# Kernel tuning notes

Hardware: AMD Instinct MI355X
Metric: run time of the kernel (lower is better)

Reference implementation:

```python
import jax, jax.numpy as jnp
import numpy as np

C = 512
NUM_GROUPS = 4
EPS = 1e-6


def _conv1x1(W, b, t):
    # 1x1x1 Conv3d == per-position linear over channels
    return jnp.einsum('oc,bcfhw->bofhw', W, t) + b[None, :, None, None, None]


def setup_inputs() -> dict:
    key = jax.random.key(0)
    ks = jax.random.split(key, 11)
    c = C
    x = jax.random.normal(ks[0], (12, c, 48, 48), dtype=jnp.float32)
    p = lambda k: jax.random.normal(k, (c, c), dtype=jnp.float32) * 0.02
    return {
        'x': x,
        'norm_scale': jnp.ones((c,), jnp.float32),
        'norm_bias': jnp.zeros((c,), jnp.float32),
        'q_w': p(ks[1]), 'q_b': jnp.zeros((c,), jnp.float32),
        'k_w': p(ks[2]), 'k_b': jnp.zeros((c,), jnp.float32),
        'v_w': p(ks[3]), 'v_b': jnp.zeros((c,), jnp.float32),
        'proj_w': p(ks[4]), 'proj_b': jnp.zeros((c,), jnp.float32),
    }


def reference(x, norm_scale, norm_bias, q_w, q_b, k_w, k_b, v_w, v_b, proj_w, proj_b):
    b3, c, h, w = x.shape
    b = b3 // 3
    # chunk batch into 3 frames, stack at frame dim -> (b, c, 3, h, w)
    h_ = jnp.stack(jnp.split(x, 3, axis=0), axis=2)
    # GroupNorm(num_groups=4) over (C/G, F, H, W) per group
    g = NUM_GROUPS
    xg = h_.reshape(b, g, c // g, 3, h, w)
    mean = jnp.mean(xg, axis=(2, 3, 4, 5), keepdims=True)
    var = jnp.var(xg, axis=(2, 3, 4, 5), keepdims=True)
    xn = ((xg - mean) * jax.lax.rsqrt(var + EPS)).reshape(b, c, 3, h, w)
    hn = xn * norm_scale[None, :, None, None, None] + norm_bias[None, :, None, None, None]
    q = _conv1x1(q_w, q_b, hn)[:, :, 1:2]          # middle frame only: (b,c,1,h,w)
    skip = q[:, :, 0]                               # (b,c,h,w)
    k = _conv1x1(k_w, k_b, hn)                      # (b,c,3,h,w)
    v = _conv1x1(v_w, v_b, hn)
    n = h * w
    qf = q.reshape(b, c, n)                         # (b,c,n)
    kf = k.reshape(b, c, 3 * n)                     # (b,c,3n)
    vf = v.reshape(b, c, 3 * n)
    scores = jnp.einsum('bcn,bcm->bnm', qf, kf) * (float(c) ** -0.5)
    attn = jax.nn.softmax(scores, axis=2)           # (b,n,3n)
    out = jnp.einsum('bcm,bnm->bcn', vf, attn).reshape(b, c, 1, h, w)
    out = _conv1x1(proj_w, proj_b, out)[:, :, 0]
    return skip + out
```

## Files before the change

kernel.cpp:

```cpp
#include <hip/hip_runtime.h>

typedef unsigned short u16;
typedef unsigned long long u64;
typedef __attribute__((ext_vector_type(8))) short short8;
typedef __attribute__((ext_vector_type(4))) float f32x4;

__device__ __forceinline__ float bf2f(u16 h) {
    union { unsigned int u; float f; } v; v.u = ((unsigned int)h) << 16; return v.f;
}
__device__ __forceinline__ u16 f2bf(float f) {
    union { float f; unsigned int u; } v; v.f = f;
    unsigned int r = v.u + 0x7fffu + ((v.u >> 16) & 1u);
    return (u16)(r >> 16);
}

__device__ __forceinline__ void gload16(const u16* g, u16* l) {
    __builtin_amdgcn_global_load_lds(
        (const __attribute__((address_space(1))) void*)g,
        (__attribute__((address_space(3))) void*)l,
        16, 0, 0);
}

__device__ __forceinline__ float waveSum(float v) {
#pragma unroll
    for (int o = 32; o > 0; o >>= 1) v += __shfl_down(v, o);
    return v;
}
__device__ __forceinline__ float waveMax(float v) {
#pragma unroll
    for (int o = 32; o > 0; o >>= 1) v = fmaxf(v, __shfl_down(v, o));
    return v;
}
__device__ __forceinline__ int waveSumI(int v) {
#pragma unroll
    for (int o = 32; o > 0; o >>= 1) v += __shfl_down(v, o);
    return v;
}

__global__ __launch_bounds__(256) void detect_k(const u16* __restrict__ x, int* __restrict__ flag) {
    __shared__ int cnt[4];
    int c = 0;
    for (int i = threadIdx.x; i < 8192; i += 256) {
        u16 e = x[i * 2];
        int ex = (e >> 7) & 0xFF;
        c += (ex == 0 || (ex >= 100 && ex <= 150)) ? 1 : 0;
    }
    c = waveSumI(c);
    if ((threadIdx.x & 63) == 0) cnt[threadIdx.x >> 6] = c;
    __syncthreads();
    if (threadIdx.x == 0)
        flag[0] = ((cnt[0] + cnt[1] + cnt[2] + cnt[3]) > 4915) ? 1 : 0;
}

__global__ __launch_bounds__(256) void conv_k(const void* __restrict__ src, u16* __restrict__ dst,
                                              int n8, const int* __restrict__ flag) {
    int i = blockIdx.x * 256 + threadIdx.x;
    if (i >= n8) return;
    if (flag[0]) {
        ((int4*)dst)[i] = ((const int4*)src)[i];
    } else {
        const float* f = (const float*)src + (size_t)i * 8;
        union { int4 v4; u16 o[8]; } tv;
#pragma unroll
        for (int j = 0; j < 8; j++) tv.o[j] = f2bf(f[j]);
        ((int4*)dst)[i] = tv.v4;
    }
}

__global__ __launch_bounds__(256) void conv_w4(const void* s0, const void* s1, const void* s2, const void* s3,
                                               u16* __restrict__ dst, const int* __restrict__ flag) {
    int i = blockIdx.x * 256 + threadIdx.x;
    int w = blockIdx.y;
    const void* s = w == 0 ? s0 : w == 1 ? s1 : w == 2 ? s2 : s3;
    u16* d = dst + (size_t)w * 262144;
    if (flag[0]) {
        ((int4*)d)[i] = ((const int4*)s)[i];
    } else {
        const float* f = (const float*)s + (size_t)i * 8;
        union { int4 v4; u16 o[8]; } tv;
#pragma unroll
        for (int j = 0; j < 8; j++) tv.o[j] = f2bf(f[j]);
        ((int4*)d)[i] = tv.v4;
    }
}

__global__ __launch_bounds__(256) void conv_v6(const void* s0, const void* s1, const void* s2,
                                               const void* s3, const void* s4, const void* s5,
                                               u16* __restrict__ dst, const int* __restrict__ flag) {
    for (int i = threadIdx.x; i < 384; i += 256) {
        int seg = i >> 6, off = i & 63;
        const void* s = seg == 0 ? s0 : seg == 1 ? s1 : seg == 2 ? s2 : seg == 3 ? s3 : seg == 4 ? s4 : s5;
        u16* d = dst + (size_t)seg * 512;
        if (flag[0]) {
            ((int4*)d)[off] = ((const int4*)s)[off];
        } else {
            const float* f = (const float*)s + (size_t)off * 8;
            union { int4 v4; u16 o[8]; } tv;
#pragma unroll
            for (int j = 0; j < 8; j++) tv.o[j] = f2bf(f[j]);
            ((int4*)d)[off] = tv.v4;
        }
    }
}

__global__ __launch_bounds__(256) void gn_stats(const u16* __restrict__ x, float* __restrict__ stat) {
    __shared__ float red[8];
    const int gg = blockIdx.y, chunk = blockIdx.x;
    const int b = gg >> 2, g = gg & 3;
    float s = 0.f, s2 = 0.f;
    for (int pp = 0; pp < 12; pp++) {
        int p = chunk * 12 + pp;
        int t = p >> 7, cc = p & 127;
        const u16* rowp = x + (size_t)((t * 4 + b) * 512 + g * 128 + cc) * 2304;
        for (int vi = threadIdx.x; vi < 288; vi += 256) {
            union { int4 v4; u16 u[8]; } tv;
            tv.v4 = *(const int4*)(rowp + vi * 8);
#pragma unroll
            for (int j = 0; j < 8; j++) { float f = bf2f(tv.u[j]); s += f; s2 += f * f; }
        }
    }
    s = waveSum(s); s2 = waveSum(s2);
    int wid = threadIdx.x >> 6;
    if ((threadIdx.x & 63) == 0) { red[wid] = s; red[wid + 4] = s2; }
    __syncthreads();
    if (threadIdx.x == 0) {
        atomicAdd(&stat[gg], red[0] + red[1] + red[2] + red[3]);
        atomicAdd(&stat[16 + gg], red[4] + red[5] + red[6] + red[7]);
    }
}

__global__ void gn_ab(const float* __restrict__ stat, const u16* __restrict__ scale,
                      const u16* __restrict__ bias, float2* __restrict__ ab) {
    int idx = blockIdx.x * 256 + threadIdx.x;
    int b = idx >> 9, c = idx & 511, g = c >> 7, gg = b * 4 + g;
    const float invN = 1.f / 884736.f;
    float mean = stat[gg] * invN;
    float var  = stat[16 + gg] * invN - mean * mean;
    float rstd = rsqrtf(var + 1e-6f);
    float a = rstd * bf2f(scale[c]);
    ab[idx] = make_float2(a, bf2f(bias[c]) - mean * a);
}

__global__ __launch_bounds__(256) void normT_k(const u16* __restrict__ xb,
                                               const float2* __restrict__ ab,
                                               u16* __restrict__ xnT) {
    __shared__ u16 t[64][72];
    const int zz = blockIdx.z;
    const int b = zz & 3, tt = zz >> 2;
    const u16* s = xb + (size_t)zz * 512 * 2304;
    u16* d = xnT + (size_t)b * (512L * 6912) + (size_t)tt * 2304 * 512;
    const int c0 = blockIdx.x * 64;
    const int r0 = blockIdx.y * 64;
    const int tid = threadIdx.x;
#pragma unroll
    for (int p = 0; p < 4; p++) {
        int r = p * 16 + (tid >> 4);
        int c4 = (tid & 15) * 4;
        float2 sab = ab[b * 512 + r0 + r];
        union { u64 u; u16 e[4]; } tv;
        tv.u = *(const u64*)(s + (size_t)(r0 + r) * 2304 + c0 + c4);
#pragma unroll
        for (int j = 0; j < 4; j++) t[r][c4 + j] = f2bf(bf2f(tv.e[j]) * sab.x + sab.y);
    }
    __syncthreads();
#pragma unroll
    for (int p = 0; p < 2; p++) {
        int n = p * 32 + (tid >> 3);
        int c8 = (tid & 7) * 8;
        union { int4 v4; u16 o[8]; } tv;
#pragma unroll
        for (int j = 0; j < 8; j++) tv.o[j] = t[c8 + j][n];
        *(int4*)(d + (size_t)(c0 + n) * 512 + r0 + c8) = tv.v4;
    }
}

template<int WR, int WC, int TI, int TJ, int AMODE, int BMODE, int EPI, int F32OUT, int SPLITK, int SWZ>
__global__ __launch_bounds__(256)
void gemm_k(const u16* __restrict__ A, const u16* __restrict__ B, void* __restrict__ Cv,
            const u16* __restrict__ bias, const u16* __restrict__ skip,
            const float2* __restrict__ ab,
            int lda, int ldb, int ldc,
            int K, float alpha, int m_off, int b0,
            long aZS, long bZS, long cZS, long sZS) {
    constexpr int BM = WR * TI * 16;
    constexpr int BN = WC * TJ * 16;
    constexpr int LDA_S = (AMODE == 0) ? 32 : 44;
    constexpr int LDB_S = (BMODE == 1) ? 32 : 44;
    __shared__ alignas(16) u16 As[2][BM][LDA_S];
    __shared__ alignas(16) u16 Bs[2][BN][LDB_S];

    int bxi = blockIdx.x, byi = blockIdx.y, bzi = blockIdx.z;
    if (SWZ) {
        int gx = gridDim.x, gy = gridDim.y;
        long NN = (long)gx * gy * gridDim.z;
        long L = bxi + (long)gx * (byi + (long)gy * bzi);
        long q = NN >> 3, r = NN & 7;
        long xc = L & 7, m = L >> 3;
        long nl = (xc < r ? xc * (q + 1) : r * (q + 1) + (xc - r) * q) + m;
        bxi = (int)(nl % gx);
        long t2 = nl / gx;
        byi = (int)(t2 % gy);
        bzi = (int)(t2 / gy);
    }

    const int tid = threadIdx.x;
    const int z = bzi;
    const int i0b = byi * BM;
    const int j0b = bxi * BN;
    const int kstart = SPLITK ? z * K : 0;

    const u16* Ap = A + (size_t)z * aZS;
    const u16* Bp;
    const float2* abp = nullptr;
    int yx0 = 0;
    if (BMODE == 2) {
        int b = b0 + (SPLITK ? 0 : z);
        int m_tile = j0b + m_off;
        int t = m_tile / 2304;
        yx0 = m_tile - t * 2304;
        Bp = B + (size_t)((t * 4 + b) * 512) * 2304;
        abp = ab + b * 512;
    } else {
        Bp = B + (size_t)z * bZS;
    }
    const u16* Sp = (EPI & 10) ? (skip + (size_t)z * sZS) : nullptr;
    float* Cf = (float*)Cv + (size_t)z * (F32OUT ? cZS : 0);
    u16*   Ch = (u16*)Cv   + (size_t)z * (F32OUT ? 0 : cZS);

    const int wave = tid >> 6;
    const int lane = tid & 63;
    const int wr = wave / WC;
    const int wc = wave % WC;
    const int lrow = lane & 15;
    const int quad = lane >> 4;
    const int sws = ((quad ^ ((lrow >> 1) & 3)) << 3);

    auto stage = [&](int bsel, int k0) {
        if (AMODE == 0) {
            constexpr int NV = (BM * 32 / 8) / 256;
#pragma unroll
            for (int v = 0; v < NV; v++) {
                int vid = tid + v * 256;
                int i = vid >> 2;
                int ks = (((vid & 3) ^ ((vid >> 3) & 3)) * 8);
                gload16(Ap + (size_t)(i0b + i) * lda + (k0 + ks), &As[bsel][i][(vid & 3) * 8]);
            }
        } else {
            constexpr int NV = (BM * 32 / 8) / 256;
            constexpr int IG = BM / 8;
#pragma unroll
            for (int v = 0; v < NV; v++) {
                int vid = tid + v * 256;
                int k = vid / IG, ib = (vid % IG) * 8;
                union { int4 v4; u16 s[8]; } tv;
                tv.v4 = *(const int4*)(Ap + (size_t)(k0 + k) * lda + (i0b + ib));
#pragma unroll
                for (int j = 0; j < 8; j++) As[bsel][ib + j][k] = tv.s[j];
            }
        }
        if (BMODE == 1) {
            constexpr int NV = (BN * 32 / 8) / 256;
#pragma unroll
            for (int v = 0; v < NV; v++) {
                int vid = tid + v * 256;
                int j = vid >> 2;
                int ks = (((vid & 3) ^ ((vid >> 3) & 3)) * 8);
                gload16(Bp + (size_t)(j0b + j) * ldb + (k0 + ks), &Bs[bsel][j][(vid & 3) * 8]);
            }
        } else {
            constexpr int NV = (BN * 32 / 8) / 256;
            constexpr int JG = BN / 8;
#pragma unroll
            for (int v = 0; v < NV; v++) {
                int vid = tid + v * 256;
                int k = vid / JG, jb = (vid % JG) * 8;
                if (BMODE == 0) {
                    union { int4 v4; u16 s[8]; } tv;
                    tv.v4 = *(const int4*)(Bp + (size_t)(k0 + k) * ldb + (j0b + jb));
#pragma unroll
                    for (int j = 0; j < 8; j++) Bs[bsel][jb + j][k] = tv.s[j];
                } else {
                    union { int4 v4; u16 s[8]; } tv;
                    tv.v4 = *(const int4*)(Bp + (size_t)(k0 + k) * 2304 + (yx0 + jb));
                    float2 amb = abp[k0 + k];
#pragma unroll
                    for (int j = 0; j < 8; j++)
                        Bs[bsel][jb + j][k] = f2bf(bf2f(tv.s[j]) * amb.x + amb.y);
                }
            }
        }
    };

    f32x4 acc[TI][TJ] = {};
    const int kend = kstart + K;

    stage(0, kstart);
    __syncthreads();

    int cur = 0;
    for (int k0 = kstart; k0 < kend; k0 += 32) {
        if (k0 + 32 < kend) stage(cur ^ 1, k0 + 32);

        union FragU { short8 v; u64 u[2]; int4 v4; };
        FragU fa[TI], fb[TJ];
#pragma unroll
        for (int ri = 0; ri < TI; ri++) {
            int r = wr * TI * 16 + ri * 16 + lrow;
            if constexpr (LDA_S == 32) {
                fa[ri].v4 = *(const int4*)(&As[cur][r][sws]);
            } else {
                fa[ri].u[0] = *(const u64*)(&As[cur][r][quad * 8]);
                fa[ri].u[1] = *(const u64*)(&As[cur][r][quad * 8 + 4]);
            }
        }
#pragma unroll
        for (int cj = 0; cj < TJ; cj++) {
            int cc2 = wc * TJ * 16 + cj * 16 + lrow;
            if constexpr (LDB_S == 32) {
                fb[cj].v4 = *(const int4*)(&Bs[cur][cc2][sws]);
            } else {
                fb[cj].u[0] = *(const u64*)(&Bs[cur][cc2][quad * 8]);
                fb[cj].u[1] = *(const u64*)(&Bs[cur][cc2][quad * 8 + 4]);
            }
        }
#pragma unroll
        for (int ri = 0; ri < TI; ri++)
#pragma unroll
            for (int cj = 0; cj < TJ; cj++)
                acc[ri][cj] = __builtin_amdgcn_mfma_f32_16x16x32_bf16(
                    fa[ri].v, fb[cj].v, acc[ri][cj], 0, 0, 0);

        __syncthreads();
        cur ^= 1;
    }

#pragma unroll
    for (int ri = 0; ri < TI; ri++) {
#pragma unroll
        for (int reg = 0; reg < 4; reg++) {
            int gi = i0b + wr * TI * 16 + ri * 16 + quad * 4 + reg;
            float bv = (EPI & 1) ? bf2f(bias[gi]) : 0.f;
#pragma unroll
            for (int cj = 0; cj < TJ; cj++) {
                int gj = j0b + wc * TJ * 16 + cj * 16 + lrow;
                float v = acc[ri][cj][reg] * alpha + bv;
                if (EPI & 4) v += bf2f(bias[gj]);
                if (EPI & 2) v += bf2f(Sp[(size_t)gi * ldc + gj]);
                if (EPI & 8) v += bf2f(Sp[(size_t)gj * 512 + gi]);
                if (F32OUT) Cf[(size_t)gi * ldc + gj] = v;
                else        Ch[(size_t)gi * ldc + gj] = f2bf(v);
            }
        }
    }
}

__global__ __launch_bounds__(256) void softmax_k(u16* __restrict__ sb, long zs) {
    __shared__ float row[6912];
    __shared__ float red[8];
    u16* p = sb + (size_t)blockIdx.y * zs + (size_t)blockIdx.x * 6912;
    const int tid = threadIdx.x;
    float mx = -3.0e38f;
    for (int vi = tid; vi < 864; vi += 256) {
        union { int4 v4; u16 u[8]; } tv;
        tv.v4 = *(const int4*)(p + vi * 8);
#pragma unroll
        for (int j = 0; j < 8; j++) { float f = bf2f(tv.u[j]); row[vi * 8 + j] = f; mx = fmaxf(mx, f); }
    }
    mx = waveMax(mx);
    if ((tid & 63) == 0) red[tid >> 6] = mx;
    __syncthreads();
    mx = fmaxf(fmaxf(red[0], red[1]), fmaxf(red[2], red[3]));
    __syncthreads();
    float sum = 0.f;
    for (int i = tid; i < 6912; i += 256) {
        float e = __expf(row[i] - mx);
        row[i] = e; sum += e;
    }
    sum = waveSum(sum);
    if ((tid & 63) == 0) red[4 + (tid >> 6)] = sum;
    __syncthreads();
    float inv = 1.f / (red[4] + red[5] + red[6] + red[7]);
    for (int vi = tid; vi < 864; vi += 256) {
        union { int4 v4; u16 u[8]; } tv;
#pragma unroll
        for (int j = 0; j < 8; j++) tv.u[j] = f2bf(row[vi * 8 + j] * inv);
        *(int4*)(p + vi * 8) = tv.v4;
    }
}

extern "C" void kernel_launch(void* const* d_in, const int* in_sizes, int n_in,
                              void* d_out, int out_size, void* d_ws, size_t ws_size,
                              hipStream_t stream) {
    float* out = (float*)d_out;

    const long QS = (long)512 * 2304;
    const long KS = (long)512 * 6912;
    const long SS = (long)2304 * 6912;
    const long PS = (long)512 * 2304;
    const float rs = 0.044194173824159216f;

    const size_t FIXED = 256 + 256 + 2048 * sizeof(float2)
                       + (size_t)14155776 * 2 + (size_t)4 * 262144 * 2 + 8192
                       + (size_t)14155776 * 2;
    const size_t PERNB = (size_t)(QS + KS + KS + QS + SS) * 2;
    int nb = 0;
    if      (ws_size >= FIXED + 4 * PERNB) nb = 4;
    else if (ws_size >= FIXED + 2 * PERNB) nb = 2;
    else if (ws_size >= FIXED + 1 * PERNB) nb = 1;

    char* w = (char*)d_ws;
    int*    flag = (int*)w;     w += 256;
    float*  stat = (float*)w;   w += 256;
    float2* ab   = (float2*)w;  w += 2048 * sizeof(float2);
    u16* xb = (u16*)w;  w += (size_t)14155776 * 2;
    u16* wgt = (u16*)w; w += (size_t)4 * 262144 * 2;
    u16* vecb = (u16*)w; w += 8192;

    detect_k<<<1, 256, 0, stream>>>((const u16*)d_in[0], flag);
    conv_k<<<6912, 256, 0, stream>>>(d_in[0], xb, 1769472, flag);
    conv_w4<<<dim3(128, 4), 256, 0, stream>>>(d_in[3], d_in[5], d_in[7], d_in[9], wgt, flag);
    conv_v6<<<1, 256, 0, stream>>>(d_in[1], d_in[2], d_in[4], d_in[6], d_in[8], d_in[10], vecb, flag);
    hipMemsetAsync(stat, 0, 32 * sizeof(float), stream);
    gn_stats<<<dim3(32, 16), 256, 0, stream>>>(xb, stat);
    gn_ab<<<8, 256, 0, stream>>>(stat, vecb, vecb + 512, ab);

    const u16* qw = wgt;
    const u16* kw = wgt + 262144;
    const u16* vw = wgt + 2 * 262144;
    const u16* pw = wgt + 3 * 262144;
    const u16* qb2 = vecb + 1024, *kb2 = vecb + 1536, *vb2 = vecb + 2048, *pb2 = vecb + 2560;

    if (nb == 0) {
        u16* qbuf = (u16*)w;  w += QS * 2;
        u16* kbuf = (u16*)w;  w += KS * 2;
        u16* vbuf = (u16*)w;  w += KS * 2;
        u16* obuf = (u16*)w;  w += QS * 2;
        u16* sbuf = (u16*)w;
        for (int b = 0; b < 4; b++) {
            gemm_k<2,2,4,4,0,2,1,0,0,0><<<dim3(54,4,1),256,0,stream>>>(
                kw, xb, kbuf, kb2, nullptr, ab, 512,0,6912, 512,1.f,0,b, 0,0,0,0);
            gemm_k<2,2,4,4,0,2,1,0,0,0><<<dim3(54,4,1),256,0,stream>>>(
                vw, xb, vbuf, vb2, nullptr, ab, 512,0,6912, 512,1.f,0,b, 0,0,0,0);
            gemm_k<2,2,4,4,0,2,1,0,0,0><<<dim3(18,4,1),256,0,stream>>>(
                qw, xb, qbuf, qb2, nullptr, ab, 512,0,2304, 512,1.f,2304,b, 0,0,0,0);
            gemm_k<2,2,4,4,1,0,0,0,0,0><<<dim3(54,18,1),256,0,stream>>>(
                qbuf, kbuf, sbuf, nullptr,nullptr,nullptr, 2304,6912,6912, 512,rs,0,b, 0,0,0,0);
            softmax_k<<<dim3(2304,1),256,0,stream>>>(sbuf, 0);
            gemm_k<1,4,4,1,0,1,0,0,0,0><<<dim3(36,8,1),256,0,stream>>>(
                vbuf, sbuf, obuf, nullptr,nullptr,nullptr, 6912,6912,2304, 6912,1.f,0,b, 0,0,0,0);
            gemm_k<2,2,4,2,0,0,3,1,0,0><<<dim3(36,4,1),256,0,stream>>>(
                pw, obuf, out + (size_t)b * PS, pb2, qbuf, nullptr,
                512,2304,2304, 512,1.f,0,b, 0,0,0,0);
        }
        return;
    }

    u16* xnT = (u16*)w; w += (size_t)14155776 * 2;
    u16* qT  = (u16*)w; w += (size_t)nb * QS * 2;
    u16* kT  = (u16*)w; w += (size_t)nb * KS * 2;
    u16* vbuf= (u16*)w; w += (size_t)nb * KS * 2;
    u16* obT = (u16*)w; w += (size_t)nb * QS * 2;
    u16* sbuf= (u16*)w; w += (size_t)nb * SS * 2;

    normT_k<<<dim3(36, 8, 12), 256, 0, stream>>>(xb, ab, xnT);

    for (int g = 0; g < 4; g += nb) {
        gemm_k<2,2,4,4,0,1,4,0,0,1><<<dim3(4,54,nb),256,0,stream>>>(
            xnT + (size_t)g * KS, kw, kT, kb2, nullptr, nullptr,
            512,512,512, 512,1.f,0,g, KS,0,KS,0);
        gemm_k<2,2,4,4,0,1,4,0,0,1><<<dim3(4,18,nb),256,0,stream>>>(
            xnT + (size_t)g * KS + (size_t)2304 * 512, qw, qT, qb2, nullptr, nullptr,
            512,512,512, 512,1.f,0,g, KS,0,QS,0);
        gemm_k<2,2,4,4,0,1,1,0,0,1><<<dim3(54,4,nb),256,0,stream>>>(
            vw, xnT + (size_t)g * KS, vbuf, vb2, nullptr, nullptr,
            512,512,6912, 512,1.f,0,g, 0,KS,KS,0);
        gemm_k<2,2,4,4,0,1,0,0,0,1><<<dim3(54,18,nb),256,0,stream>>>(
            qT, kT, sbuf, nullptr,nullptr,nullptr, 512,512,6912, 512,rs,0,g, QS,KS,SS,0);
        softmax_k<<<dim3(2304,nb),256,0,stream>>>(sbuf, SS);
        gemm_k<2,2,2,4,0,1,0,0,0,1><<<dim3(4,36,nb),256,0,stream>>>(
            sbuf, vbuf, obT, nullptr,nullptr,nullptr, 6912,6912,512, 6912,1.f,0,g, SS,KS,QS,0);
        gemm_k<2,2,4,2,0,1,9,1,0,1><<<dim3(36,4,nb),256,0,stream>>>(
            pw, obT, out + (size_t)g * PS, pb2, qT, nullptr,
            512,512,2304, 512,1.f,0,g, 0,QS,PS,QS);
    }
}
```

Baseline: 502.3 us.

## Triple-buffer GEMM LDS staging with explicit vmcnt waits for direct-load path

For GEMM variants that use direct global-to-LDS loads (AMODE 0, BMODE 1), the K loop moves to a three-buffer pipeline that keeps two tiles in flight. It waits with explicit s_waitcnt vmcnt counts and raw s_barrier instead of __syncthreads, so the next-next tile keeps loading while the current one is computed. It also raises wave priority around the MFMA block. The cost is more LDS per block, which may lower occupancy, and the hand-counted vmcnt values must match the number of loads each stage issues.

```diff
diff --git a/kernel.cpp b/kernel.cpp
--- a/kernel.cpp
+++ b/kernel.cpp
@@ -19,6 +19,23 @@
         (const __attribute__((address_space(1))) void*)g,
         (__attribute__((address_space(3))) void*)l,
         16, 0, 0);
+}
+
+template<int N> __device__ __forceinline__ void waitvm() {
+    static_assert(N >= 0 && N <= 12, "enumerate more");
+    if constexpr (N == 0)  asm volatile("s_waitcnt vmcnt(0)"  ::: "memory");
+    else if constexpr (N == 1)  asm volatile("s_waitcnt vmcnt(1)"  ::: "memory");
+    else if constexpr (N == 2)  asm volatile("s_waitcnt vmcnt(2)"  ::: "memory");
+    else if constexpr (N == 3)  asm volatile("s_waitcnt vmcnt(3)"  ::: "memory");
+    else if constexpr (N == 4)  asm volatile("s_waitcnt vmcnt(4)"  ::: "memory");
+    else if constexpr (N == 5)  asm volatile("s_waitcnt vmcnt(5)"  ::: "memory");
+    else if constexpr (N == 6)  asm volatile("s_waitcnt vmcnt(6)"  ::: "memory");
+    else if constexpr (N == 7)  asm volatile("s_waitcnt vmcnt(7)"  ::: "memory");
+    else if constexpr (N == 8)  asm volatile("s_waitcnt vmcnt(8)"  ::: "memory");
+    else if constexpr (N == 9)  asm volatile("s_waitcnt vmcnt(9)"  ::: "memory");
+    else if constexpr (N == 10) asm volatile("s_waitcnt vmcnt(10)" ::: "memory");
+    else if constexpr (N == 11) asm volatile("s_waitcnt vmcnt(11)" ::: "memory");
+    else                        asm volatile("s_waitcnt vmcnt(12)" ::: "memory");
 }
 
 __device__ __forceinline__ float waveSum(float v) {
@@ -184,10 +201,12 @@
             long aZS, long bZS, long cZS, long sZS) {
     constexpr int BM = WR * TI * 16;
     constexpr int BN = WC * TJ * 16;
+    constexpr bool PIPE = (AMODE == 0 && BMODE == 1);
+    constexpr int NBUF = PIPE ? 3 : 2;
     constexpr int LDA_S = (AMODE == 0) ? 32 : 44;
     constexpr int LDB_S = (BMODE == 1) ? 32 : 44;
-    __shared__ alignas(16) u16 As[2][BM][LDA_S];
-    __shared__ alignas(16) u16 Bs[2][BN][LDB_S];
+    __shared__ alignas(16) u16 As[NBUF][BM][LDA_S];
+    __shared__ alignas(16) u16 Bs[NBUF][BN][LDB_S];
 
     int bxi = blockIdx.x, byi = blockIdx.y, bzi = blockIdx.z;
     if (SWZ) {
@@ -292,46 +311,73 @@
     };
 
     f32x4 acc[TI][TJ] = {};
-    const int kend = kstart + K;
-
-    stage(0, kstart);
-    __syncthreads();
-
-    int cur = 0;
-    for (int k0 = kstart; k0 < kend; k0 += 32) {
-        if (k0 + 32 < kend) stage(cur ^ 1, k0 + 32);
-
+
+    auto compute = [&](int bsel) {
         union FragU { short8 v; u64 u[2]; int4 v4; };
         FragU fa[TI], fb[TJ];
 #pragma unroll
         for (int ri = 0; ri < TI; ri++) {
             int r = wr * TI * 16 + ri * 16 + lrow;
             if constexpr (LDA_S == 32) {
-                fa[ri].v4 = *(const int4*)(&As[cur][r][sws]);
+                fa[ri].v4 = *(const int4*)(&As[bsel][r][sws]);
             } else {
-                fa[ri].u[0] = *(const u64*)(&As[cur][r][quad * 8]);
-                fa[ri].u[1] = *(const u64*)(&As[cur][r][quad * 8 + 4]);
+                fa[ri].u[0] = *(const u64*)(&As[bsel][r][quad * 8]);
+                fa[ri].u[1] = *(const u64*)(&As[bsel][r][quad * 8 + 4]);
             }
         }
 #pragma unroll
         for (int cj = 0; cj < TJ; cj++) {
             int cc2 = wc * TJ * 16 + cj * 16 + lrow;
             if constexpr (LDB_S == 32) {
-                fb[cj].v4 = *(const int4*)(&Bs[cur][cc2][sws]);
+                fb[cj].v4 = *(const int4*)(&Bs[bsel][cc2][sws]);
             } else {
-                fb[cj].u[0] = *(const u64*)(&Bs[cur][cc2][quad * 8]);
-                fb[cj].u[1] = *(const u64*)(&Bs[cur][cc2][quad * 8 + 4]);
-            }
-        }
+                fb[cj].u[0] = *(const u64*)(&Bs[bsel][cc2][quad * 8]);
+                fb[cj].u[1] = *(const u64*)(&Bs[bsel][cc2][quad * 8 + 4]);
+            }
+        }
+        if constexpr (PIPE) __builtin_amdgcn_s_setprio(1);
 #pragma unroll
         for (int ri = 0; ri < TI; ri++)
 #pragma unroll
             for (int cj = 0; cj < TJ; cj++)
                 acc[ri][cj] = __builtin_amdgcn_mfma_f32_16x16x32_bf16(
                     fa[ri].v, fb[cj].v, acc[ri][cj], 0, 0, 0);
-
+        if constexpr (PIPE) __builtin_amdgcn_s_setprio(0);
+    };
+
+    const int kend = kstart + K;
+
+    if constexpr (PIPE) {
+        constexpr int LPS = (BM * 32 / 8) / 256 + (BN * 32 / 8) / 256;
+        const int NT = K / 32;
+        stage(0, kstart);
+        if (NT > 1) stage(1, kstart + 32);
+        int cur = 0;
+        for (int t = 0; t < NT; ++t) {
+            const int rem = NT - 1 - t;
+            if (rem >= 2) {
+                stage(cur == 0 ? 2 : (cur == 1 ? 0 : 1), kstart + (t + 2) * 32);
+                waitvm<2 * LPS>();
+            } else if (rem == 1) {
+                waitvm<LPS>();
+            } else {
+                waitvm<0>();
+            }
+            __builtin_amdgcn_s_barrier();
+            compute(cur);
+            __builtin_amdgcn_s_barrier();
+            cur = (cur == 2) ? 0 : cur + 1;
+        }
+    } else {
+        stage(0, kstart);
         __syncthreads();
-        cur ^= 1;
+        int cur = 0;
+        for (int k0 = kstart; k0 < kend; k0 += 32) {
+            if (k0 + 32 < kend) stage(cur ^ 1, k0 + 32);
+            compute(cur);
+            __syncthreads();
+            cur ^= 1;
+        }
     }
 
 #pragma unroll
```

Measured after the change: 520.6 us. +3.6%, slower.
